# Performance work log

Measured on AMD Instinct MI355X. Metric: run time of the kernel, lower is better.

Reference implementation:

```python
import jax, jax.numpy as jnp
import numpy as np


def _rotate_half(x):
    a, b = jnp.split(x, 2, axis=-1)
    return jnp.concatenate([-b, a], axis=-1)


def _rope_tables(L, d, dtype):
    inv = 1.0 / (10000.0 ** (jnp.arange(0, d, 2, dtype=jnp.float32) / d))
    ang = jnp.arange(L, dtype=jnp.float32)[:, None] * inv[None, :]  # (L, d/2)
    cos = jnp.repeat(jnp.cos(ang), 2, axis=-1)[None, :, None, :].astype(dtype)  # (1,L,1,d)
    sin = jnp.repeat(jnp.sin(ang), 2, axis=-1)[None, :, None, :].astype(dtype)
    return cos, sin


def setup_inputs() -> dict:
    key = jax.random.key(0)
    ks = jax.random.split(key, 7)
    B, L, D, h = 1, 1024, 768, 12
    d = D // h
    s = 0.02
    return {
        "X": jax.random.normal(ks[0], (B, L, D), jnp.float32),
        "Wq": jax.random.normal(ks[1], (D, D), jnp.float32) * s,
        "Wk": jax.random.normal(ks[2], (D, D), jnp.float32) * s,
        "Wv": jax.random.normal(ks[3], (D, D), jnp.float32) * s,
        "Wu": jax.random.normal(ks[4], (D, D), jnp.float32) * s,
        "Wg": jax.random.normal(ks[5], (3 * h, D), jnp.float32) * s,
        "Wo": jax.random.normal(ks[6], (D, D), jnp.float32) * s,
        "prior_mu": jnp.zeros((1, 1, h, d), jnp.float32),
        "prior_log_tau": jnp.zeros((1, 1, h, 1), jnp.float32),
    }


def _forward(X, Wq, Wk, Wv, Wu, Wg, Wo, prior_mu, prior_log_tau):
    B, L, D = X.shape
    h = prior_mu.shape[2]
    d = D // h
    eps = 1e-12
    # projections (torch Linear: x @ W.T, no bias)
    q = (X @ Wq.T).reshape(B, L, h, d)
    k = (X @ Wk.T).reshape(B, L, h, d)
    v = (X @ Wv.T).reshape(B, L, h, d)
    u = (X @ Wu.T).reshape(B, L, h, d)
    gate = (X @ Wg.T).reshape(B, L, h, 3)
    t = jnp.arange(1, L + 1, dtype=X.dtype).reshape(1, L, 1, 1)
    # calculate_logit (logit_type='deviation', causal)
    log_tau = jnp.exp(jnp.clip(prior_log_tau, -50.0, 30.0))
    u_sum = jnp.cumsum(u, axis=1)
    bar_u = (log_tau * prior_mu + u_sum) / (log_tau + t)
    s_i = -jnp.sum(u * bar_u, axis=-1, keepdims=True) / np.float32(np.sqrt(d))  # (B,L,h,1)
    # RoPE + L2 normalize q, k
    cos, sin = _rope_tables(L, d, X.dtype)
    q = q * cos + _rotate_half(q) * sin
    k = k * cos + _rotate_half(k) * sin
    q = q / jnp.maximum(jnp.linalg.norm(q, axis=-1, keepdims=True), eps)
    k = k / jnp.maximum(jnp.linalg.norm(k, axis=-1, keepdims=True), eps)
    # associative causal branch of compute_o
    s_max = jax.lax.stop_gradient(jnp.max(s_i, axis=1, keepdims=True))
    exp_s = jnp.exp(s_i - s_max)              # (B,L,h,1)
    E_t = jnp.cumsum(exp_s, axis=1)
    P_t = jnp.cumsum(s_i, axis=1)
    kv = jnp.einsum('blhd,blhe->blhde', k, v)  # (B,L,h,d,d)
    F_t = jnp.cumsum(exp_s[..., None] * kv, axis=1)
    G_t = jnp.cumsum(s_i[..., None] * kv, axis=1)
    H_t = jnp.cumsum(kv, axis=1)
    sig1 = jax.nn.sigmoid(gate[..., 0:1])      # (B,L,h,1)
    sigh = jax.nn.sigmoid(gate[..., 1:2])
    alpha = sigh / (E_t + eps)
    beta = (sig1 - sigh) / t
    gamma = -((beta * P_t + sigh) / t)
    M = alpha[..., None] * F_t + beta[..., None] * G_t + gamma[..., None] * H_t
    out = jnp.einsum('blhd,blhde->blhe', q, M)  # (B,L,h,d)
    # LayerNorm over head dim, eps=1e-5, no affine
    mu = jnp.mean(out, axis=-1, keepdims=True)
    var = jnp.mean(jnp.square(out - mu), axis=-1, keepdims=True)
    out = (out - mu) / jnp.sqrt(var + 1e-5)
    # output projection (dropout=0.0 -> identity)
    return out.reshape(B, L, D) @ Wo.T


def reference(X, Wq, Wk, Wv, Wu, Wg, Wo, prior_mu, prior_log_tau):
    return _forward(X, Wq, Wk, Wv, Wu, Wg, Wo, prior_mu, prior_log_tau)
```

## Files before the change

kernel.cpp:

```cpp
#include <hip/hip_runtime.h>
#include <hip/hip_bf16.h>
#include <math.h>

typedef __attribute__((ext_vector_type(8))) short bf16x8;
typedef __attribute__((ext_vector_type(4))) float f32x4;

#define SEQ 1024
#define DIM 768
#define NH 12
#define HD 64


__device__ __forceinline__ float wave_reduce_sum(float v) {
    for (int off = 1; off < 64; off <<= 1) v += __shfl_xor(v, off);
    return v;
}
__device__ __forceinline__ short f2bs(float x) {
    __hip_bfloat16 h = __float2bfloat16(x);
    return *reinterpret_cast<short*>(&h);
}
__device__ __forceinline__ float bs2f(short x) {
    __hip_bfloat16 h = *reinterpret_cast<__hip_bfloat16*>(&x);
    return (float)h;
}
__device__ __forceinline__ bf16x8 cvt8r(const float4& a, const float4& b) {
    bf16x8 r;
    r[0]=f2bs(a.x); r[1]=f2bs(a.y); r[2]=f2bs(a.z); r[3]=f2bs(a.w);
    r[4]=f2bs(b.x); r[5]=f2bs(b.y); r[6]=f2bs(b.z); r[7]=f2bs(b.w);
    return r;
}

__global__ __launch_bounds__(256, 3) void k_proj5(const float* __restrict__ X,
    const float* __restrict__ Wq, const float* __restrict__ Wk,
    const float* __restrict__ Wv, const float* __restrict__ Wu,
    const float* __restrict__ Wg,
    __hip_bfloat16* __restrict__ Qb, __hip_bfloat16* __restrict__ Kb,
    __hip_bfloat16* __restrict__ Vt, __hip_bfloat16* __restrict__ Ub,
    float* __restrict__ G)
{
    int rt = blockIdx.x, ct = blockIdx.y, mat = blockIdx.z;
    if (mat == 4 && ct != 0) return;
    if (mat == 2 && rt >= 12) return;
    if ((mat == 0 || mat == 1 || mat == 3) && ct >= 6) return;

    __shared__ short lds[24576];

    int tid = threadIdx.x;
    int wv = tid>>6, lane = tid&63, g = lane>>4, n = lane&15;
    int wn = wv;
    int sch = tid & 7, srow = tid >> 3;

    const float* Asrc; const float* Bsrc; int arow0, brow0, Brows;
    if (mat == 2) { Asrc = Wv; Bsrc = X; arow0 = rt*64; brow0 = ct*128; Brows = SEQ; }
    else {
        Asrc = X; arow0 = rt*64; brow0 = ct*128;
        Bsrc = (mat==0)?Wq:(mat==1)?Wk:(mat==3)?Wu:Wg;
        Brows = (mat==4) ? 36 : DIM;
    }

    float4 ra[2][2], rb[4][2];
    auto prefetch = [&](int k0) {
        for (int p = 0; p < 2; ++p) {
            const float* s = Asrc + (size_t)(arow0 + srow + p*32)*DIM + k0 + sch*8;
            ra[p][0] = *(const float4*)s; ra[p][1] = *(const float4*)(s + 4);
        }
        for (int p = 0; p < 4; ++p) {
            int gr = brow0 + srow + p*32; if (gr >= Brows) gr = Brows - 1;
            const float* s = Bsrc + (size_t)gr*DIM + k0 + sch*8;
            rb[p][0] = *(const float4*)s; rb[p][1] = *(const float4*)(s + 4);
        }
    };
    auto commit = [&](int buf) {
        short* Ab = lds + buf*4096;
        short* Bb = lds + 8192 + buf*8192;
        for (int p = 0; p < 2; ++p) {
            int r = srow + p*32;
            *(bf16x8*)(&Ab[(r*8 + (sch ^ (r&7)))*8]) = cvt8r(ra[p][0], ra[p][1]);
        }
        for (int p = 0; p < 4; ++p) {
            int r = srow + p*32;
            *(bf16x8*)(&Bb[(r*8 + (sch ^ (r&7)))*8]) = cvt8r(rb[p][0], rb[p][1]);
        }
    };

    f32x4 acc[4][2];
    for (int i=0;i<4;++i) for (int j=0;j<2;++j) acc[i][j] = (f32x4){0,0,0,0};

    prefetch(0);
    commit(0);
    for (int it = 0; it < 12; ++it) {
        __syncthreads();
        if (it < 11) prefetch((it+1)*64);
        int buf = it & 1;
        const short* Ab = lds + buf*4096;
        const short* Bb = lds + 8192 + buf*8192;
        for (int ks = 0; ks < 2; ++ks) {
            int q = ks*4 + g;
            bf16x8 af[4], bfr[2];
            for (int i=0;i<4;++i)
                af[i] = *(const bf16x8*)(&Ab[((i*16+n)*8 + (q ^ (n&7)))*8]);
            for (int j=0;j<2;++j)
                bfr[j] = *(const bf16x8*)(&Bb[((wn*32+j*16+n)*8 + (q ^ (n&7)))*8]);
            for (int i=0;i<4;++i)
                for (int j=0;j<2;++j)
                    acc[i][j] = __builtin_amdgcn_mfma_f32_16x16x32_bf16(af[i], bfr[j], acc[i][j], 0,0,0);
        }
        if (it < 11) commit(1 - buf);
    }
    __syncthreads();

    if (mat == 4) {
        for (int i=0;i<4;++i) for (int j=0;j<2;++j) for (int r=0;r<4;++r) {
            int row = rt*64 + i*16 + g*4 + r;
            int col = wn*32 + j*16 + n;
            if (col < 36) G[(size_t)row*36 + col] = acc[i][j][r];
        }
        return;
    }

    short* C = lds;
    for (int i=0;i<4;++i) for (int j=0;j<2;++j) for (int r=0;r<4;++r)
        C[(i*16 + g*4 + r)*128 + wn*32 + j*16 + n] = f2bs(acc[i][j][r]);
    __syncthreads();

    if (mat == 2) {
        for (int k = 0; k < 16; ++k) {
            int row = k*4 + wv;
            unsigned int v = ((const unsigned int*)C)[row*64 + lane];
            ((unsigned int*)(Vt + (size_t)(rt*64 + row)*SEQ + ct*128))[lane] = v;
        }
    } else if (mat == 3) {
        for (int k = 0; k < 32; ++k) {
            int u = k*4 + wv;
            int row = u >> 1, hsel = u & 1;
            Ub[((size_t)(2*ct + hsel)*SEQ + rt*64 + row)*HD + lane] =
                *(__hip_bfloat16*)&C[row*128 + hsel*64 + lane];
        }
    } else {
        __hip_bfloat16* dst = (mat==0) ? Qb : Kb;
        int i2 = lane >> 1;
        float inv = expf((float)i2 * (-9.210340371976184f / 32.f));
        for (int k = 0; k < 32; ++k) {
            int u = k*4 + wv;
            int row = u >> 1, hsel = u & 1;
            int l = rt*64 + row;
            float x = bs2f(C[row*128 + hsel*64 + lane]);
            float ang = (float)l * inv;
            float c = cosf(ang), s = sinf(ang);
            float p = __shfl(x, lane ^ 32);
            float rot = (lane < 32) ? -p : p;
            float y = x*c + rot*s;
            float nrm = wave_reduce_sum(y*y);
            y = y / fmaxf(sqrtf(nrm), 1e-12f);
            dst[((size_t)(2*ct + hsel)*SEQ + l)*HD + lane] = __float2bfloat16(y);
        }
    }
}

__global__ __launch_bounds__(1024) void k_scan(const __hip_bfloat16* __restrict__ Ub,
    const float* __restrict__ G, const float* __restrict__ pmu,
    const float* __restrict__ plt,
    float* __restrict__ si_, float* __restrict__ es_, float* __restrict__ al_,
    float* __restrict__ be_, float* __restrict__ ga_)
{
    int h = blockIdx.x;
    int tid = threadIdx.x, wv = tid >> 6, lane = tid & 63;
    __shared__ float sbuf[SEQ], ebuf[SEQ], g1b[SEQ], ghb[SEQ];
    __shared__ float stot[16][64];
    __shared__ float wmax[16];
    __shared__ float smax_s;

    float ltv = fminf(fmaxf(plt[h], -50.f), 30.f);
    float ltau = expf(ltv);
    float mu = pmu[h*HD + lane];

    const __hip_bfloat16* up = Ub + ((size_t)h*SEQ + wv*64)*HD + lane;
    float Ul = 0.f;
    for (int i = 0; i < 64; ++i) Ul += (float)up[(size_t)i*HD];
    stot[wv][lane] = Ul;
    __syncthreads();
    float pre = ltau * mu;
    for (int w2 = 0; w2 < wv; ++w2) pre += stot[w2][lane];
    float V = pre;
    for (int i = 0; i < 64; ++i) {
        float uv = (float)up[(size_t)i*HD];
        V += uv;
        int l = wv*64 + i;
        float bar = V / (ltau + (float)(l + 1));
        float p = wave_reduce_sum(uv * bar);
        if (lane == 0) sbuf[l] = -p * 0.125f;
    }
    __syncthreads();
    float v = sbuf[tid];
    float vm = v;
    for (int off = 1; off < 64; off <<= 1) vm = fmaxf(vm, __shfl_xor(vm, off));
    if (lane == 0) wmax[wv] = vm;
    __syncthreads();
    if (wv == 0) {
        float mm = (lane < 16) ? wmax[lane] : -1e30f;
        for (int off = 1; off < 16; off <<= 1) mm = fmaxf(mm, __shfl_xor(mm, off));
        if (lane == 0) smax_s = mm;
    }
    __syncthreads();
    float ev = expf(fminf(v - smax_s, 0.f));
    ebuf[tid] = ev;
    g1b[tid] = 1.f / (1.f + expf(-G[(size_t)tid*36 + h*3 + 0]));
    ghb[tid] = 1.f / (1.f + expf(-G[(size_t)tid*36 + h*3 + 1]));
    si_[h*SEQ + tid] = v;
    es_[h*SEQ + tid] = ev;
    __syncthreads();
    if (wv == 0) {
        int base = lane * 16;
        float se = 0.f, ss = 0.f;
        for (int i = 0; i < 16; ++i) { se += ebuf[base + i]; ss += sbuf[base + i]; }
        float pe = se, ps = ss;
        for (int off = 1; off < 64; off <<= 1) {
            float t1 = __shfl_up(pe, off), t2 = __shfl_up(ps, off);
            if (lane >= off) { pe += t1; ps += t2; }
        }
        float E = pe - se, P = ps - ss;
        for (int i = 0; i < 16; ++i) {
            int l = base + i;
            E += ebuf[l]; P += sbuf[l];
            float t = (float)(l + 1);
            float s1 = g1b[l], sh = ghb[l];
            float a = sh / (E + 1e-12f);
            float b = (s1 - sh) / t;
            float gm = -((b * P + sh) / t);
            al_[h*SEQ + l] = a;
            be_[h*SEQ + l] = b;
            ga_[h*SEQ + l] = gm;
        }
    }
}

__global__ __launch_bounds__(256) void k_attn(const __hip_bfloat16* __restrict__ Qb,
    const __hip_bfloat16* __restrict__ Kb, const __hip_bfloat16* __restrict__ Vt,
    const float* __restrict__ si_, const float* __restrict__ es_,
    const float* __restrict__ al_, const float* __restrict__ be_,
    const float* __restrict__ ga_, __hip_bfloat16* __restrict__ opre)
{
    int t = blockIdx.x, h = blockIdx.y;
    int wv = threadIdx.x >> 6, lane = threadIdx.x & 63;
    int g = lane >> 4, n = lane & 15;
    __shared__ short P[4][16*64];
    __shared__ float Op[4][16][64];
    short* Pw = P[wv];
    int m0 = t*16;
    const short* qrow = (const short*)Qb + ((size_t)h*SEQ + m0 + n)*HD + g*8;
    bf16x8 qa0 = *(const bf16x8*)qrow;
    bf16x8 qa1 = *(const bf16x8*)(qrow + 32);
    const float* al = al_ + h*SEQ;
    const float* be = be_ + h*SEQ;
    const float* ga = ga_ + h*SEQ;
    const float* es = es_ + h*SEQ;
    const float* si = si_ + h*SEQ;
    float A_[4], B_[4], G_[4];
    for (int r = 0; r < 4; ++r) {
        int m = m0 + g*4 + r;
        A_[r] = al[m]; B_[r] = be[m]; G_[r] = ga[m];
    }
    f32x4 acco[4];
    for (int et = 0; et < 4; ++et) acco[et] = (f32x4){0.f,0.f,0.f,0.f};

    int jtmax = t >> 2;
    for (int jt = wv; jt <= jtmax; jt += 4) {
        int j0 = jt*64;
        for (int ct = 0; ct < 4; ++ct) {
            const short* krow = (const short*)Kb + ((size_t)h*SEQ + j0 + ct*16 + n)*HD + g*8;
            bf16x8 kb0 = *(const bf16x8*)krow;
            bf16x8 kb1 = *(const bf16x8*)(krow + 32);
            f32x4 sacc = {0.f,0.f,0.f,0.f};
            sacc = __builtin_amdgcn_mfma_f32_16x16x32_bf16(qa0, kb0, sacc, 0, 0, 0);
            sacc = __builtin_amdgcn_mfma_f32_16x16x32_bf16(qa1, kb1, sacc, 0, 0, 0);
            int j = j0 + ct*16 + n;
            float ej = es[j], sj = si[j];
            int chunk = ct*2 + (n>>3), e = n&7;
            for (int r = 0; r < 4; ++r) {
                int m = m0 + g*4 + r;
                float w = (j <= m) ? (A_[r]*ej + B_[r]*sj + G_[r]) : 0.f;
                int ml = g*4 + r;
                Pw[ml*64 + (chunk ^ (ml&7))*8 + e] = f2bs(w * sacc[r]);
            }
        }
        const short* vb = (const short*)Vt + (size_t)h*HD*SEQ;
        for (int et = 0; et < 4; ++et) {
            for (int sub = 0; sub < 2; ++sub) {
                int q = sub*4 + g;
                bf16x8 pa = *(const bf16x8*)(&Pw[n*64 + (q ^ (n&7))*8]);
                bf16x8 vfr = *(const bf16x8*)(vb + (size_t)(et*16 + n)*SEQ + j0 + sub*32 + g*8);
                acco[et] = __builtin_amdgcn_mfma_f32_16x16x32_bf16(pa, vfr, acco[et], 0, 0, 0);
            }
        }
    }
    for (int et = 0; et < 4; ++et)
        for (int r = 0; r < 4; ++r)
            Op[wv][g*4 + r][et*16 + n] = acco[et][r];
    __syncthreads();
    for (int rr = 0; rr < 4; ++rr) {
        int row = wv*4 + rr;
        float v = Op[0][row][lane] + Op[1][row][lane] + Op[2][row][lane] + Op[3][row][lane];
        float sm = wave_reduce_sum(v);
        float sq = wave_reduce_sum(v*v);
        float mu = sm * (1.f/64.f);
        float var = fmaxf(sq * (1.f/64.f) - mu*mu, 0.f);
        float invs = rsqrtf(var + 1e-5f);
        opre[(size_t)(m0 + row)*DIM + h*HD + lane] = __float2bfloat16((v - mu) * invs);
    }
}

__global__ __launch_bounds__(256, 4) void k_oproj(const __hip_bfloat16* __restrict__ A,
    const float* __restrict__ Wo, float* __restrict__ out)
{
    int rt = blockIdx.x, ct = blockIdx.y;
    __shared__ short lds[16384];

    int tid = threadIdx.x;
    int wv = tid>>6, lane = tid&63, g = lane>>4, n = lane&15;
    int wm = wv>>1, wn = wv&1;
    int sch = tid & 7, srow = tid >> 3;

    bf16x8 raA[2]; float4 rbB[2][2];
    auto prefetch = [&](int k0) {
        for (int p = 0; p < 2; ++p) {
            raA[p] = *(const bf16x8*)((const short*)A + (size_t)(rt*64 + srow + p*32)*DIM + k0 + sch*8);
            const float* s = Wo + (size_t)(ct*64 + srow + p*32)*DIM + k0 + sch*8;
            rbB[p][0] = *(const float4*)s; rbB[p][1] = *(const float4*)(s + 4);
        }
    };
    auto commit = [&](int buf) {
        short* Ab = lds + buf*4096;
        short* Bb = lds + 8192 + buf*4096;
        for (int p = 0; p < 2; ++p) {
            int r = srow + p*32;
            *(bf16x8*)(&Ab[(r*8 + (sch ^ (r&7)))*8]) = raA[p];
            *(bf16x8*)(&Bb[(r*8 + (sch ^ (r&7)))*8]) = cvt8r(rbB[p][0], rbB[p][1]);
        }
    };

    f32x4 acc[2][2];
    for (int i=0;i<2;++i) for (int j=0;j<2;++j) acc[i][j] = (f32x4){0,0,0,0};

    prefetch(0);
    commit(0);
    for (int it = 0; it < 12; ++it) {
        __syncthreads();
        if (it < 11) prefetch((it+1)*64);
        int buf = it & 1;
        const short* Ab = lds + buf*4096;
        const short* Bb = lds + 8192 + buf*4096;
        for (int ks = 0; ks < 2; ++ks) {
            int q = ks*4 + g;
            bf16x8 af[2], bfr[2];
            for (int i=0;i<2;++i)
                af[i] = *(const bf16x8*)(&Ab[((wm*32+i*16+n)*8 + (q ^ (n&7)))*8]);
            for (int j=0;j<2;++j)
                bfr[j] = *(const bf16x8*)(&Bb[((wn*32+j*16+n)*8 + (q ^ (n&7)))*8]);
            for (int i=0;i<2;++i)
                for (int j=0;j<2;++j)
                    acc[i][j] = __builtin_amdgcn_mfma_f32_16x16x32_bf16(af[i], bfr[j], acc[i][j], 0,0,0);
        }
        if (it < 11) commit(1 - buf);
    }
    for (int i=0;i<2;++i) for (int j=0;j<2;++j) for (int r=0;r<4;++r) {
        int row = rt*64 + wm*32 + i*16 + g*4 + r;
        int col = ct*64 + wn*32 + j*16 + n;
        out[(size_t)row*DIM + col] = acc[i][j][r];
    }
}

extern "C" void kernel_launch(void* const* d_in, const int* in_sizes, int n_in,
                              void* d_out, int out_size, void* d_ws, size_t ws_size,
                              hipStream_t stream) {
    const float* X   = (const float*)d_in[0];
    const float* Wq  = (const float*)d_in[1];
    const float* Wk  = (const float*)d_in[2];
    const float* Wv  = (const float*)d_in[3];
    const float* Wu  = (const float*)d_in[4];
    const float* Wg  = (const float*)d_in[5];
    const float* Wo  = (const float*)d_in[6];
    const float* pmu = (const float*)d_in[7];
    const float* plt = (const float*)d_in[8];

    char* w = (char*)d_ws;
    __hip_bfloat16* Qb   = (__hip_bfloat16*)(w + 0);
    __hip_bfloat16* Kb   = (__hip_bfloat16*)(w + 1572864);
    __hip_bfloat16* Vt   = (__hip_bfloat16*)(w + 3145728);
    __hip_bfloat16* opre = (__hip_bfloat16*)(w + 4718592);
    float*          G    = (float*)(w + 6291456);
    float*          si_  = (float*)(w + 6438912);
    float*          es_  = si_ + NH*SEQ;
    float*          al_  = es_ + NH*SEQ;
    float*          be_  = al_ + NH*SEQ;
    float*          ga_  = be_ + NH*SEQ;
    __hip_bfloat16* Ub   = (__hip_bfloat16*)d_out;
    float*          out  = (float*)d_out;

    hipLaunchKernelGGL(k_proj5, dim3(16, 8, 5), dim3(256), 0, stream,
                       X, Wq, Wk, Wv, Wu, Wg, Qb, Kb, Vt, Ub, G);
    hipLaunchKernelGGL(k_scan, dim3(NH), dim3(1024), 0, stream,
                       Ub, G, pmu, plt, si_, es_, al_, be_, ga_);
    hipLaunchKernelGGL(k_attn, dim3(64, NH), dim3(256), 0, stream,
                       Qb, Kb, Vt, si_, es_, al_, be_, ga_, opre);
    hipLaunchKernelGGL(k_oproj, dim3(16, 12), dim3(256), 0, stream,
                       opre, Wo, out);
}
```

Measured before the change: 176.5 us.

## Pre-convert inputs to bf16 and stream GEMM tiles via global_load_lds

Adds a prep kernel that converts X and all projection weights, including Wo, from fp32 to bf16 in workspace on every call. The QKVU/gate projection and output projection kernels then load bf16 tiles straight into swizzled LDS with async global-to-LDS copies, with no register staging or in-loop conversion. This halves the bytes read per GEMM tile and frees VGPRs and issue slots in the main loop. The cost is an extra launch plus a full pass over the weights. Correctness also depends on the async LDS writes being complete before the barrier.

```diff
diff --git a/kernel.cpp b/kernel.cpp
--- a/kernel.cpp
+++ b/kernel.cpp
@@ -30,10 +30,45 @@
     return r;
 }
 
-__global__ __launch_bounds__(256, 3) void k_proj5(const float* __restrict__ X,
+__device__ __forceinline__ void async_copy16(const void* gptr, void* ldsbase, int lane) {
+#if __has_builtin(__builtin_amdgcn_global_load_lds)
+    __builtin_amdgcn_global_load_lds(
+        (const __attribute__((address_space(1))) unsigned int*)gptr,
+        (__attribute__((address_space(3))) unsigned int*)ldsbase, 16, 0, 0);
+#else
+    *(bf16x8*)((short*)ldsbase + lane*8) = *(const bf16x8*)gptr;
+#endif
+}
+
+__global__ __launch_bounds__(256) void k_prep(const float* __restrict__ X,
     const float* __restrict__ Wq, const float* __restrict__ Wk,
     const float* __restrict__ Wv, const float* __restrict__ Wu,
-    const float* __restrict__ Wg,
+    const float* __restrict__ Wg, const float* __restrict__ Wo,
+    short* __restrict__ Xb, short* __restrict__ Wqb, short* __restrict__ Wkb,
+    short* __restrict__ Wvb, short* __restrict__ Wub, short* __restrict__ Wgb,
+    short* __restrict__ Wob)
+{
+    int seg = blockIdx.y;
+    const float* src; short* dst; int n8;
+    switch (seg) {
+        case 0: src = X;  dst = Xb;  n8 = 98304; break;
+        case 1: src = Wq; dst = Wqb; n8 = 73728; break;
+        case 2: src = Wk; dst = Wkb; n8 = 73728; break;
+        case 3: src = Wv; dst = Wvb; n8 = 73728; break;
+        case 4: src = Wu; dst = Wub; n8 = 73728; break;
+        case 5: src = Wg; dst = Wgb; n8 = 3456;  break;
+        default: src = Wo; dst = Wob; n8 = 73728; break;
+    }
+    int i = blockIdx.x*256 + threadIdx.x;
+    if (i >= n8) return;
+    const float* s = src + (size_t)i*8;
+    *(bf16x8*)(dst + (size_t)i*8) = cvt8r(*(const float4*)s, *(const float4*)(s + 4));
+}
+
+__global__ __launch_bounds__(256, 3) void k_proj5(const short* __restrict__ Xb,
+    const short* __restrict__ Wqb, const short* __restrict__ Wkb,
+    const short* __restrict__ Wvb, const short* __restrict__ Wub,
+    const short* __restrict__ Wgb,
     __hip_bfloat16* __restrict__ Qb, __hip_bfloat16* __restrict__ Kb,
     __hip_bfloat16* __restrict__ Vt, __hip_bfloat16* __restrict__ Ub,
     float* __restrict__ G)
@@ -48,49 +83,42 @@
     int tid = threadIdx.x;
     int wv = tid>>6, lane = tid&63, g = lane>>4, n = lane&15;
     int wn = wv;
-    int sch = tid & 7, srow = tid >> 3;
-
-    const float* Asrc; const float* Bsrc; int arow0, brow0, Brows;
-    if (mat == 2) { Asrc = Wv; Bsrc = X; arow0 = rt*64; brow0 = ct*128; Brows = SEQ; }
+
+    const short* Asrc; const short* Bsrc; int arow0, brow0, Brows;
+    if (mat == 2) { Asrc = Wvb; Bsrc = Xb; arow0 = rt*64; brow0 = ct*128; Brows = SEQ; }
     else {
-        Asrc = X; arow0 = rt*64; brow0 = ct*128;
-        Bsrc = (mat==0)?Wq:(mat==1)?Wk:(mat==3)?Wu:Wg;
+        Asrc = Xb; arow0 = rt*64; brow0 = ct*128;
+        Bsrc = (mat==0)?Wqb:(mat==1)?Wkb:(mat==3)?Wub:Wgb;
         Brows = (mat==4) ? 36 : DIM;
     }
 
-    float4 ra[2][2], rb[4][2];
-    auto prefetch = [&](int k0) {
-        for (int p = 0; p < 2; ++p) {
-            const float* s = Asrc + (size_t)(arow0 + srow + p*32)*DIM + k0 + sch*8;
-            ra[p][0] = *(const float4*)s; ra[p][1] = *(const float4*)(s + 4);
-        }
-        for (int p = 0; p < 4; ++p) {
-            int gr = brow0 + srow + p*32; if (gr >= Brows) gr = Brows - 1;
-            const float* s = Bsrc + (size_t)gr*DIM + k0 + sch*8;
-            rb[p][0] = *(const float4*)s; rb[p][1] = *(const float4*)(s + 4);
-        }
-    };
-    auto commit = [&](int buf) {
+    auto dma_step = [&](int buf, int k0) {
         short* Ab = lds + buf*4096;
         short* Bb = lds + 8192 + buf*8192;
         for (int p = 0; p < 2; ++p) {
-            int r = srow + p*32;
-            *(bf16x8*)(&Ab[(r*8 + (sch ^ (r&7)))*8]) = cvt8r(ra[p][0], ra[p][1]);
+            int sbase = p*256 + wv*64;
+            int s = sbase + lane;
+            int r = s >> 3, c = s & 7, cl = c ^ (r & 7);
+            const short* gp = Asrc + (size_t)(arow0 + r)*DIM + k0 + cl*8;
+            async_copy16(gp, Ab + sbase*8, lane);
         }
         for (int p = 0; p < 4; ++p) {
-            int r = srow + p*32;
-            *(bf16x8*)(&Bb[(r*8 + (sch ^ (r&7)))*8]) = cvt8r(rb[p][0], rb[p][1]);
+            int sbase = p*256 + wv*64;
+            int s = sbase + lane;
+            int r = s >> 3, c = s & 7, cl = c ^ (r & 7);
+            int gr = brow0 + r; if (gr >= Brows) gr = Brows - 1;
+            const short* gp = Bsrc + (size_t)gr*DIM + k0 + cl*8;
+            async_copy16(gp, Bb + sbase*8, lane);
         }
     };
 
     f32x4 acc[4][2];
     for (int i=0;i<4;++i) for (int j=0;j<2;++j) acc[i][j] = (f32x4){0,0,0,0};
 
-    prefetch(0);
-    commit(0);
+    dma_step(0, 0);
     for (int it = 0; it < 12; ++it) {
         __syncthreads();
-        if (it < 11) prefetch((it+1)*64);
+        if (it < 11) dma_step(1 - (it & 1), (it + 1)*64);
         int buf = it & 1;
         const short* Ab = lds + buf*4096;
         const short* Bb = lds + 8192 + buf*8192;
@@ -105,7 +133,6 @@
                 for (int j=0;j<2;++j)
                     acc[i][j] = __builtin_amdgcn_mfma_f32_16x16x32_bf16(af[i], bfr[j], acc[i][j], 0,0,0);
         }
-        if (it < 11) commit(1 - buf);
     }
     __syncthreads();
 
@@ -309,8 +336,8 @@
     }
 }
 
-__global__ __launch_bounds__(256, 4) void k_oproj(const __hip_bfloat16* __restrict__ A,
-    const float* __restrict__ Wo, float* __restrict__ out)
+__global__ __launch_bounds__(256, 4) void k_oproj(const short* __restrict__ A,
+    const short* __restrict__ Wob, float* __restrict__ out)
 {
     int rt = blockIdx.x, ct = blockIdx.y;
     __shared__ short lds[16384];
@@ -318,34 +345,28 @@
     int tid = threadIdx.x;
     int wv = tid>>6, lane = tid&63, g = lane>>4, n = lane&15;
     int wm = wv>>1, wn = wv&1;
-    int sch = tid & 7, srow = tid >> 3;
-
-    bf16x8 raA[2]; float4 rbB[2][2];
-    auto prefetch = [&](int k0) {
-        for (int p = 0; p < 2; ++p) {
-            raA[p] = *(const bf16x8*)((const short*)A + (size_t)(rt*64 + srow + p*32)*DIM + k0 + sch*8);
-            const float* s = Wo + (size_t)(ct*64 + srow + p*32)*DIM + k0 + sch*8;
-            rbB[p][0] = *(const float4*)s; rbB[p][1] = *(const float4*)(s + 4);
-        }
-    };
-    auto commit = [&](int buf) {
+
+    auto dma_step = [&](int buf, int k0) {
         short* Ab = lds + buf*4096;
         short* Bb = lds + 8192 + buf*4096;
         for (int p = 0; p < 2; ++p) {
-            int r = srow + p*32;
-            *(bf16x8*)(&Ab[(r*8 + (sch ^ (r&7)))*8]) = raA[p];
-            *(bf16x8*)(&Bb[(r*8 + (sch ^ (r&7)))*8]) = cvt8r(rbB[p][0], rbB[p][1]);
+            int sbase = p*256 + wv*64;
+            int s = sbase + lane;
+            int r = s >> 3, c = s & 7, cl = c ^ (r & 7);
+            const short* ga_ = A + (size_t)(rt*64 + r)*DIM + k0 + cl*8;
+            async_copy16(ga_, Ab + sbase*8, lane);
+            const short* gb = Wob + (size_t)(ct*64 + r)*DIM + k0 + cl*8;
+            async_copy16(gb, Bb + sbase*8, lane);
         }
     };
 
     f32x4 acc[2][2];
     for (int i=0;i<2;++i) for (int j=0;j<2;++j) acc[i][j] = (f32x4){0,0,0,0};
 
-    prefetch(0);
-    commit(0);
+    dma_step(0, 0);
     for (int it = 0; it < 12; ++it) {
         __syncthreads();
-        if (it < 11) prefetch((it+1)*64);
+        if (it < 11) dma_step(1 - (it & 1), (it + 1)*64);
         int buf = it & 1;
         const short* Ab = lds + buf*4096;
         const short* Bb = lds + 8192 + buf*4096;
@@ -360,7 +381,6 @@
                 for (int j=0;j<2;++j)
                     acc[i][j] = __builtin_amdgcn_mfma_f32_16x16x32_bf16(af[i], bfr[j], acc[i][j], 0,0,0);
         }
-        if (it < 11) commit(1 - buf);
     }
     for (int i=0;i<2;++i) for (int j=0;j<2;++j) for (int r=0;r<4;++r) {
         int row = rt*64 + wm*32 + i*16 + g*4 + r;
@@ -393,15 +413,24 @@
     float*          al_  = es_ + NH*SEQ;
     float*          be_  = al_ + NH*SEQ;
     float*          ga_  = be_ + NH*SEQ;
+    short*          Xb   = (short*)(w + 6684672);
+    short*          Wqb  = (short*)(w + 8257536);
+    short*          Wkb  = (short*)(w + 9437184);
+    short*          Wvb  = (short*)(w + 10616832);
+    short*          Wub  = (short*)(w + 11796480);
+    short*          Wgb  = (short*)(w + 12976128);
+    short*          Wob  = (short*)(w + 13031424);
     __hip_bfloat16* Ub   = (__hip_bfloat16*)d_out;
     float*          out  = (float*)d_out;
 
+    hipLaunchKernelGGL(k_prep, dim3(384, 7), dim3(256), 0, stream,
+                       X, Wq, Wk, Wv, Wu, Wg, Wo, Xb, Wqb, Wkb, Wvb, Wub, Wgb, Wob);
     hipLaunchKernelGGL(k_proj5, dim3(16, 8, 5), dim3(256), 0, stream,
-                       X, Wq, Wk, Wv, Wu, Wg, Qb, Kb, Vt, Ub, G);
+                       Xb, Wqb, Wkb, Wvb, Wub, Wgb, Qb, Kb, Vt, Ub, G);
     hipLaunchKernelGGL(k_scan, dim3(NH), dim3(1024), 0, stream,
                        Ub, G, pmu, plt, si_, es_, al_, be_, ga_);
     hipLaunchKernelGGL(k_attn, dim3(64, NH), dim3(256), 0, stream,
                        Qb, Kb, Vt, si_, es_, al_, be_, ga_, opre);
     hipLaunchKernelGGL(k_oproj, dim3(16, 12), dim3(256), 0, stream,
-                       opre, Wo, out);
-}
+                       (const short*)opre, Wob, out);
+}
```

Measured after the change: 172.9 us. 2.0% less time.
